# Performance work log

Measured on AMD Instinct MI355X. Metric: run time of the kernel, lower is better.

The kernel has to match this reference:

```python
import jax, jax.numpy as jnp
import numpy as np
import math

MAXL = 3
TAUS = [16, 16, 16, 16]
OUT_TAUS = [16, 16, 16, 16]
BM_CNT = 1.0
BM_EPS = 1e-5

# (l1, l2, l) triples in the kernel's triple-loop order, bucketed by output l
TRIPLES = {l: [] for l in range(MAXL + 1)}
for _l1 in range(MAXL + 1):
    for _l2 in range(_l1 + 1):
        for _l in range(_l1 - _l2, min(_l1 + _l2, MAXL) + 1):
            TRIPLES[_l].append((_l1, _l2))

MIDDLE_TAUS = [sum(TAUS[a] * TAUS[b] for (a, b) in TRIPLES[l]) for l in range(MAXL + 1)]


def _cg_coef(l1, m1, l2, m2, l, m):
    if m1 + m2 != m:
        return 0.0
    f = math.factorial
    pre = math.sqrt((2 * l + 1) * f(l1 + l2 - l) * f(l1 - l2 + l) * f(-l1 + l2 + l) / f(l1 + l2 + l + 1))
    pre *= math.sqrt(f(l + m) * f(l - m) * f(l1 - m1) * f(l1 + m1) * f(l2 - m2) * f(l2 + m2))
    s = 0.0
    for k in range(0, l1 + l2 - l + 1):
        d = [k, l1 + l2 - l - k, l1 - m1 - k, l2 + m2 - k, l - l2 + m1 + k, l - l1 - m2 + k]
        if any(x < 0 for x in d):
            continue
        den = 1.0
        for x in d:
            den *= f(x)
        s += (-1.0) ** k / den
    return pre * s


def _cg_tensor(l1, l2, l):
    t = np.zeros((2 * l1 + 1, 2 * l2 + 1, 2 * l + 1), dtype=np.float32)
    for i, m1 in enumerate(range(-l1, l1 + 1)):
        for j, m2 in enumerate(range(-l2, l2 + 1)):
            m = m1 + m2
            if -l <= m <= l:
                t[i, j, m + l] = _cg_coef(l1, m1, l2, m2, l, m)
    return t

CG = {}
for _l in range(MAXL + 1):
    for (_l1, _l2) in TRIPLES[_l]:
        CG[(_l1, _l2, _l)] = jnp.asarray(_cg_tensor(_l1, _l2, _l))

# complex-multiply contraction tensor: (a*b)[k] = a[i] b[j] CM[i,j,k]
_CM = np.zeros((2, 2, 2), dtype=np.float32)
_CM[0, 0, 0] = 1.0; _CM[1, 1, 0] = -1.0; _CM[0, 1, 1] = 1.0; _CM[1, 0, 1] = 1.0
CM = jnp.asarray(_CM)


def setup_inputs() -> dict:
    key = jax.random.key(0)
    k1, k2, k3 = jax.random.split(key, 3)
    in_len = sum(TAUS[l] * (2 * l + 1) for l in range(MAXL + 1))  # 256
    wlen = sum(OUT_TAUS[l] * MIDDLE_TAUS[l] for l in range(MAXL + 1))  # 90112
    activations = jax.random.normal(k1, (2048, in_len, 2), dtype=jnp.float32)
    W = 0.05 * jax.random.uniform(k2, (wlen, 2), dtype=jnp.float32)
    bn_stds = jax.random.uniform(k3, (sum(MIDDLE_TAUS),), dtype=jnp.float32)
    return {"activations": activations, "W": W, "bn_stds": bn_stds}


def reference(activations, W, bn_stds):
    B = activations.shape[0]
    # split input into per-l parts: [B, tau_l, 2l+1, 2]
    Fs = []
    st = 0
    for l in range(MAXL + 1):
        ln = TAUS[l] * (2 * l + 1)
        Fs.append(activations[:, st:st + ln, :].reshape(B, TAUS[l], 2 * l + 1, 2))
        st += ln
    outs = []
    w_st = 0
    s_st = 0
    for l in range(MAXL + 1):
        # Clebsch-Gordan products feeding output degree l
        mids = []
        for (l1, l2) in TRIPLES[l]:
            c = jnp.einsum('btmi,bsnj,mnp,ijk->btspk', Fs[l1], Fs[l2], CG[(l1, l2, l)], CM)
            mids.append(c.reshape(B, TAUS[l1] * TAUS[l2], 2 * l + 1, 2))
        mid = jnp.concatenate(mids, axis=1)  # [B, M_l, 2l+1, 2]
        Ml = MIDDLE_TAUS[l]
        # fused batchnorm: per-middle-channel std over batch and m, moving average update
        batch_std = jnp.sqrt(jnp.mean(jnp.sum(mid * mid, axis=-1), axis=(0, 2)))  # [M_l]
        mov = bn_stds[s_st:s_st + Ml]
        new_std = (mov * BM_CNT + batch_std) / (BM_CNT + 1.0)
        mid = mid / (new_std + BM_EPS)[None, :, None, None]
        # complex linear mix over middle channels -> out_taus[l]
        wl = jax.lax.dynamic_slice_in_dim(W, w_st, OUT_TAUS[l] * Ml, axis=0).reshape(OUT_TAUS[l], Ml, 2)
        out_l = jnp.einsum('oci,bcmj,ijk->bomk', wl, mid, CM)
        outs.append(out_l.reshape(B, OUT_TAUS[l] * (2 * l + 1), 2))
        w_st += OUT_TAUS[l] * Ml
        s_st += Ml
    return jnp.concatenate(outs, axis=1)  # [B, 256, 2]
```

## Files before the change

kernel.cpp:

```cpp
#include <hip/hip_runtime.h>
#include <math.h>

typedef __attribute__((ext_vector_type(8))) short bf16x8;
typedef __attribute__((ext_vector_type(4))) float f32x4;

constexpr double cfact(int n){ double r=1.0; for(int i=2;i<=n;++i) r*=(double)i; return r; }
constexpr double csqrt_(double x){ double g=(x>1.0)?x:1.0; for(int i=0;i<100;++i) g=0.5*(g+x/g); return g; }
constexpr double cg_coef_(int l1,int m1,int l2,int m2,int l,int m){
  double pre = csqrt_((double)(2*l+1)*cfact(l1+l2-l)*cfact(l1-l2+l)*cfact(-l1+l2+l)/cfact(l1+l2+l+1));
  pre = pre*csqrt_(cfact(l+m)*cfact(l-m)*cfact(l1-m1)*cfact(l1+m1)*cfact(l2-m2)*cfact(l2+m2));
  double s=0.0;
  for(int k=0;k<=l1+l2-l;++k){
    int d0=k,d1=l1+l2-l-k,d2=l1-m1-k,d3=l2+m2-k,d4=l-l2+m1+k,d5=l-l1-m2+k;
    if(d0<0||d1<0||d2<0||d3<0||d4<0||d5<0) continue;
    double den=cfact(d0)*cfact(d1)*cfact(d2)*cfact(d3)*cfact(d4)*cfact(d5);
    s+=((k&1)?-1.0:1.0)/den;
  }
  return pre*s;
}
struct CGList{ int n; float coef[64]; int mi[64]; int ni[64]; int pi[64]; };
constexpr CGList build_cg(int l1,int l2,int l){
  CGList T{};
  for(int i=0;i<2*l1+1;++i){
    for(int j=0;j<2*l2+1;++j){
      int m1=i-l1, m2=j-l2, m=m1+m2;
      if(m<-l||m>l) continue;
      double c=cg_coef_(l1,m1,l2,m2,l,m);
      if(c>1e-12||c<-1e-12){
        T.coef[T.n]=(float)c; T.mi[T.n]=i; T.ni[T.n]=j; T.pi[T.n]=m+l; T.n++;
      }
    }
  }
  return T;
}

__device__ __host__ constexpr int AOFF(int l){ return l==0?0: l==1?16: l==2?64:144; }
__device__ __host__ constexpr int MLs(int l){ return l==0?1024: l==1?1536: l==2?1792:1536; }
__device__ __host__ constexpr int WOFF(int l){ return l==0?0: l==1?16384: l==2?40960:69632; }
__device__ __host__ constexpr int SOFF(int l){ return l==0?0: l==1?1024: l==2?2560:4352; }
__device__ __host__ constexpr int ABASE(int l){ return l==0?0: l==1?65536: l==2?163840:278528; }

#define DEVFN __device__ __forceinline__
#define BP 68
#define AP 68

DEVFN unsigned f2bf2(float x, float y){
  unsigned ux = __float_as_uint(x); ux = (ux + 0x7FFFu + ((ux>>16)&1u)) >> 16;
  unsigned uy = __float_as_uint(y); uy = (uy + 0x7FFFu + ((uy>>16)&1u)) >> 16;
  return (ux & 0xFFFFu) | (uy << 16);
}

template<int L1,int L2,int L>
DEVFN void cg_accum(const float2* F1, const float2* F2, float2* mid){
  constexpr CGList T = build_cg(L1,L2,L);
  #pragma unroll
  for(int e=0;e<T.n;++e){
    const float c = T.coef[e];
    const float2 a = F1[T.mi[e]];
    const float2 b = F2[T.ni[e]];
    float pr = a.x*b.x - a.y*b.y;
    float pim= a.x*b.y + a.y*b.x;
    mid[T.pi[e]].x += c*pr;
    mid[T.pi[e]].y += c*pim;
  }
}

template<int L1,int L2,int L>
DEVFN void k1c(const float2* F1, const float2* F2a, const float2* F2b,
               float& ssa, float& ssb){
  constexpr int NP=2*L+1;
  float2 mida[NP], midb[NP];
  #pragma unroll
  for(int p=0;p<NP;++p){ mida[p]=make_float2(0.f,0.f); midb[p]=make_float2(0.f,0.f); }
  cg_accum<L1,L2,L>(F1,F2a,mida);
  cg_accum<L1,L2,L>(F1,F2b,midb);
  #pragma unroll
  for(int p=0;p<NP;++p){
    ssa += mida[p].x*mida[p].x + mida[p].y*mida[p].y;
    ssb += midb[p].x*midb[p].x + midb[p].y*midb[p].y;
  }
}

template<int L1,int L2,int L>
DEVFN void k1g(const float2* __restrict__ act2, int b0, int u, int bh,
               float& ssa, float& ssb){
  constexpr int N1=2*L1+1, N2=2*L2+1;
  const int t = u>>3, s0 = (u&7)*2;
  const float2* base1  = act2 + AOFF(L1) + t*N1;
  const float2* base2a = act2 + AOFF(L2) + s0*N2;
  const float2* base2b = base2a + N2;
  float2 F1c[N1], F2ac[N2], F2bc[N2];
  float2 F1n[N1], F2an[N2], F2bn[N2];
  {
    const size_t ro = (size_t)(b0 + bh*16)*256;
    #pragma unroll
    for(int m=0;m<N1;++m) F1c[m]=base1[ro+m];
    #pragma unroll
    for(int n=0;n<N2;++n){ F2ac[n]=base2a[ro+n]; F2bc[n]=base2b[ro+n]; }
  }
  #pragma unroll
  for(int bi=0;bi<16;bi+=2){
    {
      const size_t ro = (size_t)(b0 + bh*16 + bi + 1)*256;
      #pragma unroll
      for(int m=0;m<N1;++m) F1n[m]=base1[ro+m];
      #pragma unroll
      for(int n=0;n<N2;++n){ F2an[n]=base2a[ro+n]; F2bn[n]=base2b[ro+n]; }
    }
    k1c<L1,L2,L>(F1c,F2ac,F2bc,ssa,ssb);
    if(bi+2<16){
      const size_t ro = (size_t)(b0 + bh*16 + bi + 2)*256;
      #pragma unroll
      for(int m=0;m<N1;++m) F1c[m]=base1[ro+m];
      #pragma unroll
      for(int n=0;n<N2;++n){ F2ac[n]=base2a[ro+n]; F2bc[n]=base2b[ro+n]; }
    }
    k1c<L1,L2,L>(F1n,F2an,F2bn,ssa,ssb);
  }
}

DEVFN void convW(const float* __restrict__ W, short* __restrict__ A, int idx){
  int l = (idx<1024)?0 : (idx<2560)?1 : (idx<4352)?2 : 3;
  int c = idx - SOFF(l);
  int Ml = MLs(l);
  const float2* wbase = (const float2*)W + WOFF(l) + c;
  unsigned* Aw = (unsigned*)(A + ABASE(l));
  #pragma unroll 4
  for(int o=0;o<16;++o){
    float2 w = wbase[(size_t)o*Ml];
    Aw[(size_t)o*Ml + c]      = f2bf2(w.x, -w.y);
    Aw[(size_t)(o+16)*Ml + c] = f2bf2(w.y,  w.x);
  }
}

__global__ __launch_bounds__(256) void k_sumsq(const float* __restrict__ act,
                                               float2* __restrict__ part,
                                               const float* __restrict__ W,
                                               short* __restrict__ A){
  const int bid = blockIdx.x;
  const int tid = threadIdx.x;
  if(bid >= 1472){
    convW(W, A, (bid-1472)*256 + tid);
    return;
  }
  const int order[23] = {22,16,21,18,15,20,13,9,14,8,17,7,12,6,10,3,5,19,2,11,1,4,0};
  const int ti = order[bid>>6];
  const int chunk = bid&63;
  const int b0 = chunk*32;
  const int u = tid & 127, bh = tid >> 7;
  const float2* act2 = (const float2*)act;
  float ssa=0.f, ssb=0.f;
  switch(ti){
    case 0:  k1g<0,0,0>(act2,b0,u,bh,ssa,ssb); break;
    case 1:  k1g<1,1,0>(act2,b0,u,bh,ssa,ssb); break;
    case 2:  k1g<2,2,0>(act2,b0,u,bh,ssa,ssb); break;
    case 3:  k1g<3,3,0>(act2,b0,u,bh,ssa,ssb); break;
    case 4:  k1g<1,0,1>(act2,b0,u,bh,ssa,ssb); break;
    case 5:  k1g<1,1,1>(act2,b0,u,bh,ssa,ssb); break;
    case 6:  k1g<2,1,1>(act2,b0,u,bh,ssa,ssb); break;
    case 7:  k1g<2,2,1>(act2,b0,u,bh,ssa,ssb); break;
    case 8:  k1g<3,2,1>(act2,b0,u,bh,ssa,ssb); break;
    case 9:  k1g<3,3,1>(act2,b0,u,bh,ssa,ssb); break;
    case 10: k1g<1,1,2>(act2,b0,u,bh,ssa,ssb); break;
    case 11: k1g<2,0,2>(act2,b0,u,bh,ssa,ssb); break;
    case 12: k1g<2,1,2>(act2,b0,u,bh,ssa,ssb); break;
    case 13: k1g<2,2,2>(act2,b0,u,bh,ssa,ssb); break;
    case 14: k1g<3,1,2>(act2,b0,u,bh,ssa,ssb); break;
    case 15: k1g<3,2,2>(act2,b0,u,bh,ssa,ssb); break;
    case 16: k1g<3,3,2>(act2,b0,u,bh,ssa,ssb); break;
    case 17: k1g<2,1,3>(act2,b0,u,bh,ssa,ssb); break;
    case 18: k1g<2,2,3>(act2,b0,u,bh,ssa,ssb); break;
    case 19: k1g<3,0,3>(act2,b0,u,bh,ssa,ssb); break;
    case 20: k1g<3,1,3>(act2,b0,u,bh,ssa,ssb); break;
    case 21: k1g<3,2,3>(act2,b0,u,bh,ssa,ssb); break;
    default: k1g<3,3,3>(act2,b0,u,bh,ssa,ssb); break;
  }
  part[(size_t)((ti*64 + chunk)*2 + bh)*128 + u] = make_float2(ssa, ssb);
}

__global__ __launch_bounds__(256) void k_scale(const float* __restrict__ bn,
                                               const float2* __restrict__ part,
                                               float* __restrict__ s){
  const int ti = blockIdx.x;
  const int ch = threadIdx.x;
  const int idx = ti*256 + ch;
  const int u = ch>>1;
  const float2* ps = part + (size_t)ti*128*128 + u;
  float sum = 0.f;
  #pragma unroll 8
  for(int r=0;r<128;++r){
    float2 v = ps[(size_t)r*128];
    sum += (ch&1) ? v.y : v.x;
  }
  int l = (idx<1024)?0 : (idx<2560)?1 : (idx<4352)?2 : 3;
  float divi = (l==0)?(1.f/2048.f) : (l==1)?(1.f/6144.f) : (l==2)?(1.f/10240.f) : (1.f/14336.f);
  float bstd = sqrtf(sum*divi);
  float nstd = 0.5f*(bn[idx]+bstd);
  s[idx] = 1.f/(nstd+1e-5f);
}


#define BT_B   0
#define LA_B   17408

template<int NTIL>
DEVFN void kf_pre(char* smem){
  const int tid = threadIdx.x;
  unsigned* btile = (unsigned*)(smem + BT_B);
  for(int i=tid; i<NTIL*16*BP; i+=256) btile[i]=0;
  __syncthreads();
}

template<int L1,int L2,int L,int Q,int NTIL>
DEVFN void kf_triple(const float2* __restrict__ act2, int b0, char* smem,
                     const unsigned* __restrict__ Aw,
                     const float* __restrict__ sg, f32x4& cR, f32x4& cI){
  constexpr int N1=2*L1+1, N2=2*L2+1, NP=2*L+1;
  constexpr int Ml = MLs(L);
  unsigned* btile  = (unsigned*)(smem + BT_B);
  unsigned* ldsA   = (unsigned*)(smem + LA_B);
  const int tid = threadIdx.x;
  const int lane = tid & 63, w = tid >> 6;
  const int col = lane & 15, quad = lane >> 4;
  const int up = tid & 31, bi = tid >> 5;
  const int r0 = tid>>4,       j0 = (tid&15)*4;
  const int r1 = (tid+256)>>4;
  const float2* arow = act2 + (size_t)(b0+bi)*256;
  uint4 v0 = *(const uint4*)(Aw + (size_t)r0*Ml + Q*256 + j0);
  uint4 v1 = *(const uint4*)(Aw + (size_t)r1*Ml + Q*256 + j0);
  #pragma unroll 1
  for(int cc=0; cc<4; ++cc){
    {
      const float2 s2 = *(const float2*)(sg + SOFF(L) + Q*256 + cc*64 + 2*up);
      const int u = cc*32 + up;
      const int t = u>>3, s0 = (u&7)*2;
      float2 F1[N1], F2a[N2], F2b[N2], mida[NP], midb[NP];
      #pragma unroll
      for(int m=0;m<N1;++m) F1[m]=arow[AOFF(L1)+t*N1+m];
      #pragma unroll
      for(int n=0;n<N2;++n){
        F2a[n]=arow[AOFF(L2)+s0*N2+n];
        F2b[n]=arow[AOFF(L2)+(s0+1)*N2+n];
      }
      #pragma unroll
      for(int p=0;p<NP;++p){ mida[p]=make_float2(0.f,0.f); midb[p]=make_float2(0.f,0.f); }
      cg_accum<L1,L2,L>(F1,F2a,mida);
      cg_accum<L1,L2,L>(F1,F2b,midb);
      #pragma unroll
      for(int p=0;p<NP;++p){
        uint2 v;
        v.x = f2bf2(mida[p].x*s2.x, mida[p].y*s2.x);
        v.y = f2bf2(midb[p].x*s2.y, midb[p].y*s2.y);
        *(uint2*)(btile + (size_t)(bi*NP+p)*BP + 2*up) = v;
      }
    }
    *(uint4*)(ldsA + r0*AP + j0) = v0;
    *(uint4*)(ldsA + r1*AP + j0) = v1;
    if(cc<3){
      const int base = Q*256 + (cc+1)*64;
      v0 = *(const uint4*)(Aw + (size_t)r0*Ml + base + j0);
      v1 = *(const uint4*)(Aw + (size_t)r1*Ml + base + j0);
    }
    __syncthreads();
    if(w < NTIL){
      const unsigned* ar0 = ldsA + col*AP + quad*4;
      const unsigned* ar1 = ldsA + (col+16)*AP + quad*4;
      const unsigned* bb  = btile + (w*16+col)*BP + quad*4;
      #pragma unroll
      for(int ks=0; ks<4; ++ks){
        bf16x8 b  = *(const bf16x8*)(bb + ks*16);
        bf16x8 A0 = *(const bf16x8*)(ar0 + ks*16);
        bf16x8 A1 = *(const bf16x8*)(ar1 + ks*16);
        cR = __builtin_amdgcn_mfma_f32_16x16x32_bf16(A0, b, cR, 0, 0, 0);
        cI = __builtin_amdgcn_mfma_f32_16x16x32_bf16(A1, b, cI, 0, 0, 0);
      }
    }
    __syncthreads();
  }
}

template<int L,int NTIL>
DEVFN void kf_epi(float* __restrict__ out, int b0, f32x4 cR, f32x4 cI){
  constexpr int NP = 2*L+1;
  const int tid = threadIdx.x, lane = tid & 63, w = tid >> 6;
  const int col = lane & 15, quad = lane >> 4;
  if(w < NTIL){
    const int r = w*16 + col;
    if(r < 8*NP){
      const int b = b0 + r/NP, p = r - (r/NP)*NP;
      float2* o2 = (float2*)out + (size_t)b*256 + AOFF(L);
      #pragma unroll
      for(int i=0;i<4;++i) o2[(quad*4+i)*NP + p] = make_float2(cR[i], cI[i]);
    }
  }
}

__global__ __launch_bounds__(256,3) void k_fusedall(const float* __restrict__ act,
    const short* __restrict__ A, const float* __restrict__ sg,
    float* __restrict__ out){
  __shared__ __align__(16) char smem[26112];
  const int bid = blockIdx.x;
  const float2* act2 = (const float2*)act;
  f32x4 cR={0.f,0.f,0.f,0.f}, cI={0.f,0.f,0.f,0.f};
  if(bid < 256){
    const int b0 = bid*8;
    kf_pre<4>(smem);
    const unsigned* Aw=(const unsigned*)(A+ABASE(3));
    kf_triple<2,1,3,0,4>(act2,b0,smem,Aw,sg,cR,cI);
    kf_triple<2,2,3,1,4>(act2,b0,smem,Aw,sg,cR,cI);
    kf_triple<3,0,3,2,4>(act2,b0,smem,Aw,sg,cR,cI);
    kf_triple<3,1,3,3,4>(act2,b0,smem,Aw,sg,cR,cI);
    kf_triple<3,2,3,4,4>(act2,b0,smem,Aw,sg,cR,cI);
    kf_triple<3,3,3,5,4>(act2,b0,smem,Aw,sg,cR,cI);
    kf_epi<3,4>(out,b0,cR,cI);
  } else if(bid < 512){
    const int b0 = (bid-256)*8;
    kf_pre<3>(smem);
    const unsigned* Aw=(const unsigned*)(A+ABASE(2));
    kf_triple<1,1,2,0,3>(act2,b0,smem,Aw,sg,cR,cI);
    kf_triple<2,0,2,1,3>(act2,b0,smem,Aw,sg,cR,cI);
    kf_triple<2,1,2,2,3>(act2,b0,smem,Aw,sg,cR,cI);
    kf_triple<2,2,2,3,3>(act2,b0,smem,Aw,sg,cR,cI);
    kf_triple<3,1,2,4,3>(act2,b0,smem,Aw,sg,cR,cI);
    kf_triple<3,2,2,5,3>(act2,b0,smem,Aw,sg,cR,cI);
    kf_triple<3,3,2,6,3>(act2,b0,smem,Aw,sg,cR,cI);
    kf_epi<2,3>(out,b0,cR,cI);
  } else if(bid < 768){
    const int b0 = (bid-512)*8;
    kf_pre<2>(smem);
    const unsigned* Aw=(const unsigned*)(A+ABASE(1));
    kf_triple<1,0,1,0,2>(act2,b0,smem,Aw,sg,cR,cI);
    kf_triple<1,1,1,1,2>(act2,b0,smem,Aw,sg,cR,cI);
    kf_triple<2,1,1,2,2>(act2,b0,smem,Aw,sg,cR,cI);
    kf_triple<2,2,1,3,2>(act2,b0,smem,Aw,sg,cR,cI);
    kf_triple<3,2,1,4,2>(act2,b0,smem,Aw,sg,cR,cI);
    kf_triple<3,3,1,5,2>(act2,b0,smem,Aw,sg,cR,cI);
    kf_epi<1,2>(out,b0,cR,cI);
  } else {
    const int b0 = (bid-768)*8;
    kf_pre<1>(smem);
    const unsigned* Aw=(const unsigned*)(A+ABASE(0));
    kf_triple<0,0,0,0,1>(act2,b0,smem,Aw,sg,cR,cI);
    kf_triple<1,1,0,1,1>(act2,b0,smem,Aw,sg,cR,cI);
    kf_triple<2,2,0,2,1>(act2,b0,smem,Aw,sg,cR,cI);
    kf_triple<3,3,0,3,1>(act2,b0,smem,Aw,sg,cR,cI);
    kf_epi<0,1>(out,b0,cR,cI);
  }
}

extern "C" void kernel_launch(void* const* d_in, const int* in_sizes, int n_in,
                              void* d_out, int out_size, void* d_ws, size_t ws_size,
                              hipStream_t stream) {
  const float* act = (const float*)d_in[0];
  const float* W   = (const float*)d_in[1];
  const float* bn  = (const float*)d_in[2];
  float* out = (float*)d_out;

  float*  s    = (float*)d_ws;
  short*  A    = (short*)((char*)d_ws + 24576);
  float2* part = (float2*)((char*)d_ws + 1048576);

  hipLaunchKernelGGL(k_sumsq,   dim3(1495), dim3(256), 0, stream, act, part, W, A);
  hipLaunchKernelGGL(k_scale,   dim3(23),   dim3(256), 0, stream, bn, part, s);
  hipLaunchKernelGGL(k_fusedall,dim3(1024), dim3(256), 0, stream, act, A, s, out);
}
```

Baseline: 143.8 us.

## Split heavy l=3 and l=2 triple work across extra blocks with atomic accumulation

The l=3 and l=2 output groups, which carry the most Clebsch-Gordan triples, are each split over two sets of blocks, and every set handles a subset of the triples. Partial results are combined with float atomicAdd into an output buffer that is zeroed by a memset first. The grid grows from 1024 to 1536 blocks to balance the per-block load and cut the tail set by the slowest blocks. The cost is an extra memset, atomic traffic, and summation order that is no longer deterministic.

Result: slower. 160.1 us (+11.3%).

```diff
diff --git a/kernel.cpp b/kernel.cpp
--- a/kernel.cpp
+++ b/kernel.cpp
@@ -279,7 +279,7 @@
   }
 }
 
-template<int L,int NTIL>
+template<int L,int NTIL,bool ATOMIC>
 DEVFN void kf_epi(float* __restrict__ out, int b0, f32x4 cR, f32x4 cI){
   constexpr int NP = 2*L+1;
   const int tid = threadIdx.x, lane = tid & 63, w = tid >> 6;
@@ -288,9 +288,19 @@
     const int r = w*16 + col;
     if(r < 8*NP){
       const int b = b0 + r/NP, p = r - (r/NP)*NP;
-      float2* o2 = (float2*)out + (size_t)b*256 + AOFF(L);
-      #pragma unroll
-      for(int i=0;i<4;++i) o2[(quad*4+i)*NP + p] = make_float2(cR[i], cI[i]);
+      if(ATOMIC){
+        float* ob = out + ((size_t)b*256 + AOFF(L) + p)*2;
+        #pragma unroll
+        for(int i=0;i<4;++i){
+          const int o = quad*4 + i;
+          atomicAdd(ob + (size_t)o*NP*2,     cR[i]);
+          atomicAdd(ob + (size_t)o*NP*2 + 1, cI[i]);
+        }
+      } else {
+        float2* o2 = (float2*)out + (size_t)b*256 + AOFF(L);
+        #pragma unroll
+        for(int i=0;i<4;++i) o2[(quad*4+i)*NP + p] = make_float2(cR[i], cI[i]);
+      }
     }
   }
 }
@@ -306,27 +316,37 @@
     const int b0 = bid*8;
     kf_pre<4>(smem);
     const unsigned* Aw=(const unsigned*)(A+ABASE(3));
+    kf_triple<3,3,3,5,4>(act2,b0,smem,Aw,sg,cR,cI);
+    kf_triple<3,2,3,4,4>(act2,b0,smem,Aw,sg,cR,cI);
+    kf_epi<3,4,true>(out,b0,cR,cI);
+  } else if(bid < 512){
+    const int b0 = (bid-256)*8;
+    kf_pre<4>(smem);
+    const unsigned* Aw=(const unsigned*)(A+ABASE(3));
     kf_triple<2,1,3,0,4>(act2,b0,smem,Aw,sg,cR,cI);
     kf_triple<2,2,3,1,4>(act2,b0,smem,Aw,sg,cR,cI);
     kf_triple<3,0,3,2,4>(act2,b0,smem,Aw,sg,cR,cI);
     kf_triple<3,1,3,3,4>(act2,b0,smem,Aw,sg,cR,cI);
-    kf_triple<3,2,3,4,4>(act2,b0,smem,Aw,sg,cR,cI);
-    kf_triple<3,3,3,5,4>(act2,b0,smem,Aw,sg,cR,cI);
-    kf_epi<3,4>(out,b0,cR,cI);
-  } else if(bid < 512){
-    const int b0 = (bid-256)*8;
+    kf_epi<3,4,true>(out,b0,cR,cI);
+  } else if(bid < 768){
+    const int b0 = (bid-512)*8;
+    kf_pre<3>(smem);
+    const unsigned* Aw=(const unsigned*)(A+ABASE(2));
+    kf_triple<3,3,2,6,3>(act2,b0,smem,Aw,sg,cR,cI);
+    kf_triple<3,2,2,5,3>(act2,b0,smem,Aw,sg,cR,cI);
+    kf_triple<2,0,2,1,3>(act2,b0,smem,Aw,sg,cR,cI);
+    kf_epi<2,3,true>(out,b0,cR,cI);
+  } else if(bid < 1024){
+    const int b0 = (bid-768)*8;
     kf_pre<3>(smem);
     const unsigned* Aw=(const unsigned*)(A+ABASE(2));
     kf_triple<1,1,2,0,3>(act2,b0,smem,Aw,sg,cR,cI);
-    kf_triple<2,0,2,1,3>(act2,b0,smem,Aw,sg,cR,cI);
     kf_triple<2,1,2,2,3>(act2,b0,smem,Aw,sg,cR,cI);
     kf_triple<2,2,2,3,3>(act2,b0,smem,Aw,sg,cR,cI);
     kf_triple<3,1,2,4,3>(act2,b0,smem,Aw,sg,cR,cI);
-    kf_triple<3,2,2,5,3>(act2,b0,smem,Aw,sg,cR,cI);
-    kf_triple<3,3,2,6,3>(act2,b0,smem,Aw,sg,cR,cI);
-    kf_epi<2,3>(out,b0,cR,cI);
-  } else if(bid < 768){
-    const int b0 = (bid-512)*8;
+    kf_epi<2,3,true>(out,b0,cR,cI);
+  } else if(bid < 1280){
+    const int b0 = (bid-1024)*8;
     kf_pre<2>(smem);
     const unsigned* Aw=(const unsigned*)(A+ABASE(1));
     kf_triple<1,0,1,0,2>(act2,b0,smem,Aw,sg,cR,cI);
@@ -335,16 +355,16 @@
     kf_triple<2,2,1,3,2>(act2,b0,smem,Aw,sg,cR,cI);
     kf_triple<3,2,1,4,2>(act2,b0,smem,Aw,sg,cR,cI);
     kf_triple<3,3,1,5,2>(act2,b0,smem,Aw,sg,cR,cI);
-    kf_epi<1,2>(out,b0,cR,cI);
+    kf_epi<1,2,false>(out,b0,cR,cI);
   } else {
-    const int b0 = (bid-768)*8;
+    const int b0 = (bid-1280)*8;
     kf_pre<1>(smem);
     const unsigned* Aw=(const unsigned*)(A+ABASE(0));
     kf_triple<0,0,0,0,1>(act2,b0,smem,Aw,sg,cR,cI);
     kf_triple<1,1,0,1,1>(act2,b0,smem,Aw,sg,cR,cI);
     kf_triple<2,2,0,2,1>(act2,b0,smem,Aw,sg,cR,cI);
     kf_triple<3,3,0,3,1>(act2,b0,smem,Aw,sg,cR,cI);
-    kf_epi<0,1>(out,b0,cR,cI);
+    kf_epi<0,1,false>(out,b0,cR,cI);
   }
 }
 
@@ -360,7 +380,8 @@
   short*  A    = (short*)((char*)d_ws + 24576);
   float2* part = (float2*)((char*)d_ws + 1048576);
 
+  hipMemsetAsync(out, 0, (size_t)2048*256*2*sizeof(float), stream);
   hipLaunchKernelGGL(k_sumsq,   dim3(1495), dim3(256), 0, stream, act, part, W, A);
   hipLaunchKernelGGL(k_scale,   dim3(23),   dim3(256), 0, stream, bn, part, s);
-  hipLaunchKernelGGL(k_fusedall,dim3(1024), dim3(256), 0, stream, act, A, s, out);
-}
+  hipLaunchKernelGGL(k_fusedall,dim3(1536), dim3(256), 0, stream, act, A, s, out);
+}
```

## Split l=2,3 blocks to 4 batch rows with wider K chunks

Applied to the files above, without the earlier changes.

For output degrees 2 and 3, each block now handles 4 batch rows instead of 8, which doubles the number of blocks for the heaviest degrees and raises the grid from 1024 to 1536. A new triple routine has each thread compute two middle channels and processes 256 middle channels per stage in two 128-wide K chunks of 8 MFMA steps on 2 waves. The intent is to balance work across CUs and reduce the tail from the heavy l=3 blocks. The cost is more LDS per block, which may limit occupancy, and fewer active MFMA waves per block.

New measurement: 148.5 us. +3.3%, slower.

```diff
diff --git a/kernel.cpp b/kernel.cpp
--- a/kernel.cpp
+++ b/kernel.cpp
@@ -43,6 +43,8 @@
 #define DEVFN __device__ __forceinline__
 #define BP 68
 #define AP 68
+#define BP4 132
+#define AP4 132
 
 DEVFN unsigned f2bf2(float x, float y){
   unsigned ux = __float_as_uint(x); ux = (ux + 0x7FFFu + ((ux>>16)&1u)) >> 16;
@@ -202,12 +204,21 @@
 
 #define BT_B   0
 #define LA_B   17408
+#define BT4_B  0
+#define LA4_B  16896
 
 template<int NTIL>
 DEVFN void kf_pre(char* smem){
   const int tid = threadIdx.x;
   unsigned* btile = (unsigned*)(smem + BT_B);
   for(int i=tid; i<NTIL*16*BP; i+=256) btile[i]=0;
+  __syncthreads();
+}
+
+DEVFN void kf_pre4(char* smem){
+  const int tid = threadIdx.x;
+  unsigned* btile = (unsigned*)(smem + BT4_B);
+  for(int i=tid; i<32*BP4; i+=256) btile[i]=0;
   __syncthreads();
 }
 
@@ -279,14 +290,90 @@
   }
 }
 
-template<int L,int NTIL>
+template<int L1,int L2,int L,int Q>
+DEVFN void kf_triple4(const float2* __restrict__ act2, int b0, char* smem,
+                      const unsigned* __restrict__ Aw,
+                      const float* __restrict__ sg, f32x4& cR, f32x4& cI){
+  constexpr int N1=2*L1+1, N2=2*L2+1, NP=2*L+1;
+  constexpr int Ml = MLs(L);
+  unsigned* btile  = (unsigned*)(smem + BT4_B);
+  unsigned* ldsA   = (unsigned*)(smem + LA4_B);
+  const int tid = threadIdx.x;
+  const int lane = tid & 63, w = tid >> 6;
+  const int col = lane & 15, quad = lane >> 4;
+  const int up = tid & 31;
+  const int bi = (tid >> 5) & 3;
+  const int ch2 = tid >> 7;
+  const int ar = tid >> 4;
+  const int aj = (tid & 15) * 8;
+  const float2* arow = act2 + (size_t)(b0+bi)*256;
+  uint4 v0 = *(const uint4*)(Aw + (size_t)ar*Ml      + Q*256 + aj);
+  uint4 v1 = *(const uint4*)(Aw + (size_t)ar*Ml      + Q*256 + aj + 4);
+  uint4 v2 = *(const uint4*)(Aw + (size_t)(ar+16)*Ml + Q*256 + aj);
+  uint4 v3 = *(const uint4*)(Aw + (size_t)(ar+16)*Ml + Q*256 + aj + 4);
+  #pragma unroll 1
+  for(int it=0; it<2; ++it){
+    {
+      const int u = it*64 + ch2*32 + up;
+      const float2 s2 = *(const float2*)(sg + SOFF(L) + Q*256 + 2*u);
+      const int t = u>>3, s0 = (u&7)*2;
+      float2 F1[N1], F2a[N2], F2b[N2], mida[NP], midb[NP];
+      #pragma unroll
+      for(int m=0;m<N1;++m) F1[m]=arow[AOFF(L1)+t*N1+m];
+      #pragma unroll
+      for(int n=0;n<N2;++n){
+        F2a[n]=arow[AOFF(L2)+s0*N2+n];
+        F2b[n]=arow[AOFF(L2)+(s0+1)*N2+n];
+      }
+      #pragma unroll
+      for(int p=0;p<NP;++p){ mida[p]=make_float2(0.f,0.f); midb[p]=make_float2(0.f,0.f); }
+      cg_accum<L1,L2,L>(F1,F2a,mida);
+      cg_accum<L1,L2,L>(F1,F2b,midb);
+      #pragma unroll
+      for(int p=0;p<NP;++p){
+        uint2 v;
+        v.x = f2bf2(mida[p].x*s2.x, mida[p].y*s2.x);
+        v.y = f2bf2(midb[p].x*s2.y, midb[p].y*s2.y);
+        *(uint2*)(btile + (size_t)(bi*NP+p)*BP4 + ch2*64 + 2*up) = v;
+      }
+    }
+    *(uint4*)(ldsA + ar*AP4      + aj)     = v0;
+    *(uint4*)(ldsA + ar*AP4      + aj + 4) = v1;
+    *(uint4*)(ldsA + (ar+16)*AP4 + aj)     = v2;
+    *(uint4*)(ldsA + (ar+16)*AP4 + aj + 4) = v3;
+    if(it==0){
+      const int base = Q*256 + 128;
+      v0 = *(const uint4*)(Aw + (size_t)ar*Ml      + base + aj);
+      v1 = *(const uint4*)(Aw + (size_t)ar*Ml      + base + aj + 4);
+      v2 = *(const uint4*)(Aw + (size_t)(ar+16)*Ml + base + aj);
+      v3 = *(const uint4*)(Aw + (size_t)(ar+16)*Ml + base + aj + 4);
+    }
+    __syncthreads();
+    if(w < 2){
+      const unsigned* ar0 = ldsA + col*AP4 + quad*4;
+      const unsigned* ar1 = ldsA + (col+16)*AP4 + quad*4;
+      const unsigned* bb  = btile + (w*16+col)*BP4 + quad*4;
+      #pragma unroll
+      for(int ks=0; ks<8; ++ks){
+        bf16x8 b  = *(const bf16x8*)(bb + ks*16);
+        bf16x8 A0 = *(const bf16x8*)(ar0 + ks*16);
+        bf16x8 A1 = *(const bf16x8*)(ar1 + ks*16);
+        cR = __builtin_amdgcn_mfma_f32_16x16x32_bf16(A0, b, cR, 0, 0, 0);
+        cI = __builtin_amdgcn_mfma_f32_16x16x32_bf16(A1, b, cI, 0, 0, 0);
+      }
+    }
+    __syncthreads();
+  }
+}
+
+template<int L,int NTIL,int B>
 DEVFN void kf_epi(float* __restrict__ out, int b0, f32x4 cR, f32x4 cI){
   constexpr int NP = 2*L+1;
   const int tid = threadIdx.x, lane = tid & 63, w = tid >> 6;
   const int col = lane & 15, quad = lane >> 4;
   if(w < NTIL){
     const int r = w*16 + col;
-    if(r < 8*NP){
+    if(r < B*NP){
       const int b = b0 + r/NP, p = r - (r/NP)*NP;
       float2* o2 = (float2*)out + (size_t)b*256 + AOFF(L);
       #pragma unroll
@@ -298,35 +385,35 @@
 __global__ __launch_bounds__(256,3) void k_fusedall(const float* __restrict__ act,
     const short* __restrict__ A, const float* __restrict__ sg,
     float* __restrict__ out){
-  __shared__ __align__(16) char smem[26112];
+  __shared__ __align__(16) char smem[33792];
   const int bid = blockIdx.x;
   const float2* act2 = (const float2*)act;
   f32x4 cR={0.f,0.f,0.f,0.f}, cI={0.f,0.f,0.f,0.f};
-  if(bid < 256){
-    const int b0 = bid*8;
-    kf_pre<4>(smem);
+  if(bid < 512){
+    const int b0 = bid*4;
+    kf_pre4(smem);
     const unsigned* Aw=(const unsigned*)(A+ABASE(3));
-    kf_triple<2,1,3,0,4>(act2,b0,smem,Aw,sg,cR,cI);
-    kf_triple<2,2,3,1,4>(act2,b0,smem,Aw,sg,cR,cI);
-    kf_triple<3,0,3,2,4>(act2,b0,smem,Aw,sg,cR,cI);
-    kf_triple<3,1,3,3,4>(act2,b0,smem,Aw,sg,cR,cI);
-    kf_triple<3,2,3,4,4>(act2,b0,smem,Aw,sg,cR,cI);
-    kf_triple<3,3,3,5,4>(act2,b0,smem,Aw,sg,cR,cI);
-    kf_epi<3,4>(out,b0,cR,cI);
-  } else if(bid < 512){
-    const int b0 = (bid-256)*8;
-    kf_pre<3>(smem);
+    kf_triple4<2,1,3,0>(act2,b0,smem,Aw,sg,cR,cI);
+    kf_triple4<2,2,3,1>(act2,b0,smem,Aw,sg,cR,cI);
+    kf_triple4<3,0,3,2>(act2,b0,smem,Aw,sg,cR,cI);
+    kf_triple4<3,1,3,3>(act2,b0,smem,Aw,sg,cR,cI);
+    kf_triple4<3,2,3,4>(act2,b0,smem,Aw,sg,cR,cI);
+    kf_triple4<3,3,3,5>(act2,b0,smem,Aw,sg,cR,cI);
+    kf_epi<3,2,4>(out,b0,cR,cI);
+  } else if(bid < 1024){
+    const int b0 = (bid-512)*4;
+    kf_pre4(smem);
     const unsigned* Aw=(const unsigned*)(A+ABASE(2));
-    kf_triple<1,1,2,0,3>(act2,b0,smem,Aw,sg,cR,cI);
-    kf_triple<2,0,2,1,3>(act2,b0,smem,Aw,sg,cR,cI);
-    kf_triple<2,1,2,2,3>(act2,b0,smem,Aw,sg,cR,cI);
-    kf_triple<2,2,2,3,3>(act2,b0,smem,Aw,sg,cR,cI);
-    kf_triple<3,1,2,4,3>(act2,b0,smem,Aw,sg,cR,cI);
-    kf_triple<3,2,2,5,3>(act2,b0,smem,Aw,sg,cR,cI);
-    kf_triple<3,3,2,6,3>(act2,b0,smem,Aw,sg,cR,cI);
-    kf_epi<2,3>(out,b0,cR,cI);
-  } else if(bid < 768){
-    const int b0 = (bid-512)*8;
+    kf_triple4<1,1,2,0>(act2,b0,smem,Aw,sg,cR,cI);
+    kf_triple4<2,0,2,1>(act2,b0,smem,Aw,sg,cR,cI);
+    kf_triple4<2,1,2,2>(act2,b0,smem,Aw,sg,cR,cI);
+    kf_triple4<2,2,2,3>(act2,b0,smem,Aw,sg,cR,cI);
+    kf_triple4<3,1,2,4>(act2,b0,smem,Aw,sg,cR,cI);
+    kf_triple4<3,2,2,5>(act2,b0,smem,Aw,sg,cR,cI);
+    kf_triple4<3,3,2,6>(act2,b0,smem,Aw,sg,cR,cI);
+    kf_epi<2,2,4>(out,b0,cR,cI);
+  } else if(bid < 1280){
+    const int b0 = (bid-1024)*8;
     kf_pre<2>(smem);
     const unsigned* Aw=(const unsigned*)(A+ABASE(1));
     kf_triple<1,0,1,0,2>(act2,b0,smem,Aw,sg,cR,cI);
@@ -335,16 +422,16 @@
     kf_triple<2,2,1,3,2>(act2,b0,smem,Aw,sg,cR,cI);
     kf_triple<3,2,1,4,2>(act2,b0,smem,Aw,sg,cR,cI);
     kf_triple<3,3,1,5,2>(act2,b0,smem,Aw,sg,cR,cI);
-    kf_epi<1,2>(out,b0,cR,cI);
+    kf_epi<1,2,8>(out,b0,cR,cI);
   } else {
-    const int b0 = (bid-768)*8;
+    const int b0 = (bid-1280)*8;
     kf_pre<1>(smem);
     const unsigned* Aw=(const unsigned*)(A+ABASE(0));
     kf_triple<0,0,0,0,1>(act2,b0,smem,Aw,sg,cR,cI);
     kf_triple<1,1,0,1,1>(act2,b0,smem,Aw,sg,cR,cI);
     kf_triple<2,2,0,2,1>(act2,b0,smem,Aw,sg,cR,cI);
     kf_triple<3,3,0,3,1>(act2,b0,smem,Aw,sg,cR,cI);
-    kf_epi<0,1>(out,b0,cR,cI);
+    kf_epi<0,1,8>(out,b0,cR,cI);
   }
 }
 
@@ -356,11 +443,11 @@
   const float* bn  = (const float*)d_in[2];
   float* out = (float*)d_out;
 
-  float*  s    = (float*)d_ws;
-  short*  A    = (short*)((char*)d_ws + 24576);
-  float2* part = (float2*)((char*)d_ws + 1048576);
+  float*    s    = (float*)d_ws;
+  short*    A    = (short*)((char*)d_ws + 24576);
+  float2*   part = (float2*)((char*)d_ws + 1048576);
 
   hipLaunchKernelGGL(k_sumsq,   dim3(1495), dim3(256), 0, stream, act, part, W, A);
   hipLaunchKernelGGL(k_scale,   dim3(23),   dim3(256), 0, stream, bn, part, s);
-  hipLaunchKernelGGL(k_fusedall,dim3(1024), dim3(256), 0, stream, act, A, s, out);
-}
+  hipLaunchKernelGGL(k_fusedall,dim3(1536), dim3(256), 0, stream, act, A, s, out);
+}
```
